# Kernel tuning notes

Hardware: AMD Instinct MI355X
Metric: run time of the kernel (lower is better)

The kernel has to match this reference:

```python
import jax, jax.numpy as jnp
import numpy as np

L, T, DIN, DOUT = 64, 8192, 128, 128

def setup_inputs() -> dict:
    key = jax.random.key(0)
    k1, k2, k3 = jax.random.split(key, 3)
    x = jax.random.normal(k1, (L, T, DIN), dtype=jnp.float32)
    w = jax.random.normal(k2, (L, DIN, DOUT), dtype=jnp.float32)
    b = jax.random.normal(k3, (L, 1, DOUT), dtype=jnp.float32)
    return {"x": x, "w": w, "b": b}

def reference(x, w, b):
    # grouped GEMM: per-layer matmul x[l] @ w[l], fused bias add
    out = jnp.einsum('lti,lio->lto', x, w) + b  # [L, T, DOUT]
    return out
```

## Files before the change

kernel.cpp:

```cpp
#include <hip/hip_runtime.h>
#include <hip/hip_bf16.h>

#define L_N 64
#define T_N 8192
#define K_N 128
#define N_N 128
#define BM  64

typedef __attribute__((ext_vector_type(8))) short short8;
typedef __attribute__((ext_vector_type(4))) float f32x4;

__device__ __forceinline__ unsigned short f2bf(float f) {
    union { float f; unsigned u; } c; c.f = f;
    return (unsigned short)((c.u + 0x7fffu + ((c.u >> 16) & 1u)) >> 16);
}

__global__ __launch_bounds__(256) void wfrag_kernel(const float* __restrict__ w,
                                                    unsigned short* __restrict__ wf) {
    __shared__ float lds[K_N * 129];
    const int l = blockIdx.x;
    const float* wl = w + (size_t)l * (K_N * N_N);
    const int tid = threadIdx.x;
    #pragma unroll
    for (int i = 0; i < 16; ++i) {
        int f = i * 256 + tid;
        float4 v = ((const float4*)wl)[f];
        int k = f >> 5, n = (f & 31) * 4;
        lds[k * 129 + n + 0] = v.x;
        lds[k * 129 + n + 1] = v.y;
        lds[k * 129 + n + 2] = v.z;
        lds[k * 129 + n + 3] = v.w;
    }
    __syncthreads();
    unsigned short* o = wf + (size_t)l * (N_N * K_N);
    #pragma unroll
    for (int c = 0; c < 16; ++c) {
        int chunk = c * 256 + tid;
        int j0   = (chunk & 1) * 4;
        int lane = (chunk >> 1) & 63;
        int kk   = (chunk >> 7) & 3;
        int ni   = chunk >> 9;
        int n  = ni * 16 + (lane & 15);
        int kb = kk * 32 + (lane >> 4) * 8 + j0;
        ushort4 ov;
        ov.x = f2bf(lds[(kb + 0) * 129 + n]);
        ov.y = f2bf(lds[(kb + 1) * 129 + n]);
        ov.z = f2bf(lds[(kb + 2) * 129 + n]);
        ov.w = f2bf(lds[(kb + 3) * 129 + n]);
        ((ushort4*)o)[chunk] = ov;
    }
}

__global__ __launch_bounds__(512, 6) void gl_kernel(const float* __restrict__ x,
                                                    const unsigned short* __restrict__ wf,
                                                    const float* __restrict__ bias,
                                                    float* __restrict__ out) {
    __shared__ __align__(16) char smem[49152];
    unsigned short* xs  = (unsigned short*)smem;
    unsigned short* wsh = (unsigned short*)(smem + 16384);

    const int tid  = threadIdx.x;
    const int lane = tid & 63;
    const int wid  = tid >> 6;
    const int lr   = lane & 15;
    const int lg   = lane >> 4;
    const int ws   = wid >> 1;
    const int ch   = wid & 1;

    const int bid  = blockIdx.x;
    const int l    = bid >> 7;
    const int tile = bid & 127;
    const float* xg = x + ((size_t)l * T_N + (size_t)tile * BM) * K_N;
    const unsigned short* wl = wf + (size_t)l * (N_N * K_N);

    #pragma unroll
    for (int i = 0; i < 4; ++i) {
        int f = i * 512 + tid;
        const float4 v = ((const float4*)xg)[f];
        int row = f >> 5;
        int kc  = (f & 31) * 4;
        union { unsigned short s[4]; unsigned long long u; } p;
        p.s[0] = f2bf(v.x); p.s[1] = f2bf(v.y); p.s[2] = f2bf(v.z); p.s[3] = f2bf(v.w);
        int us = (row * K_N + kc) ^ ((row & 7) << 3);
        *(unsigned long long*)&xs[us] = p.u;
    }
    #pragma unroll
    for (int i = 0; i < 4; ++i) {
        int c = i * 512 + tid;
        ((short8*)wsh)[c] = ((const short8*)wl)[c];
    }
    __syncthreads();

    f32x4 acc[4];
    #pragma unroll
    for (int q = 0; q < 4; ++q)
        acc[q] = (f32x4){0.f, 0.f, 0.f, 0.f};
    const int row = ws * 16 + lr;
    #pragma unroll
    for (int kk = 0; kk < 4; ++kk) {
        const short8 xb = *(const short8*)&xs[(row * K_N + kk * 32 + lg * 8) ^ ((row & 7) << 3)];
        #pragma unroll
        for (int q = 0; q < 4; ++q) {
            const int ni = ch * 4 + q;
            const short8 wv = ((const short8*)wsh)[(ni * 4 + kk) * 64 + lane];
            acc[q] = __builtin_amdgcn_mfma_f32_16x16x32_bf16(wv, xb, acc[q], 0, 0, 0);
        }
    }
    __syncthreads();

    const float* bl = bias + l * N_N;
    float4* osm = (float4*)(smem + wid * 4096);
    #pragma unroll
    for (int q = 0; q < 4; ++q) {
        const int ni = ch * 4 + q;
        const float4 bv = *(const float4*)(bl + ni * 16 + lg * 4);
        float4 r;
        r.x = acc[q][0] + bv.x;
        r.y = acc[q][1] + bv.y;
        r.z = acc[q][2] + bv.z;
        r.w = acc[q][3] + bv.w;
        osm[lr * 16 + ((q * 4 + lg) ^ lr)] = r;
    }
    float4* og4 = (float4*)(out + ((size_t)l * T_N + (size_t)tile * BM + ws * 16) * N_N);
    #pragma unroll
    for (int q2 = 0; q2 < 4; ++q2) {
        const int fi = q2 * 64 + lane;
        const int rr = fi >> 4, cc = fi & 15;
        const float4 v = osm[rr * 16 + (cc ^ rr)];
        og4[(size_t)rr * 32 + ch * 16 + cc] = v;
    }
}

extern "C" void kernel_launch(void* const* d_in, const int* in_sizes, int n_in,
                              void* d_out, int out_size, void* d_ws, size_t ws_size,
                              hipStream_t stream) {
    const float* x = (const float*)d_in[0];
    const float* w = (const float*)d_in[1];
    const float* b = (const float*)d_in[2];
    float* out = (float*)d_out;
    unsigned short* wf = (unsigned short*)d_ws;

    wfrag_kernel<<<L_N, 256, 0, stream>>>(w, wf);
    gl_kernel<<<L_N * (T_N / BM), 512, 0, stream>>>(x, wf, b, out);
}
```

Baseline: 105.8 us.

## Split output columns across two blocks per tile and remap block order

Each block now computes only half of the 128 output columns for a 64-row tile, which doubles the grid and halves the per-block weight load, LDS footprint and accumulators. Launch bounds rise to 8 blocks per CU, and block IDs are permuted so that consecutive blocks are spread across layers and tiles, possibly to match the XCD scheduling. The cost is that every x tile is now loaded from global memory and converted to bf16 twice, which adds read traffic to a memory-bound kernel.

```diff
diff --git a/kernel.cpp b/kernel.cpp
--- a/kernel.cpp
+++ b/kernel.cpp
@@ -51,11 +51,11 @@
     }
 }
 
-__global__ __launch_bounds__(512, 6) void gl_kernel(const float* __restrict__ x,
+__global__ __launch_bounds__(512, 8) void gl_kernel(const float* __restrict__ x,
                                                     const unsigned short* __restrict__ wf,
                                                     const float* __restrict__ bias,
                                                     float* __restrict__ out) {
-    __shared__ __align__(16) char smem[49152];
+    __shared__ __align__(16) char smem[32768];
     unsigned short* xs  = (unsigned short*)smem;
     unsigned short* wsh = (unsigned short*)(smem + 16384);
 
@@ -65,13 +65,15 @@
     const int lr   = lane & 15;
     const int lg   = lane >> 4;
     const int ws   = wid >> 1;
-    const int ch   = wid & 1;
+    const int cq   = wid & 1;
 
-    const int bid  = blockIdx.x;
-    const int l    = bid >> 7;
-    const int tile = bid & 127;
+    const int work = (blockIdx.x & 7) * 2048 + (blockIdx.x >> 3);
+    const int l    = work >> 8;
+    const int tile = (work & 255) >> 1;
+    const int ch   = work & 1;
+
     const float* xg = x + ((size_t)l * T_N + (size_t)tile * BM) * K_N;
-    const unsigned short* wl = wf + (size_t)l * (N_N * K_N);
+    const unsigned short* wl = wf + (size_t)l * (N_N * K_N) + (size_t)ch * 4 * 4 * 64 * 8;
 
     #pragma unroll
     for (int i = 0; i < 4; ++i) {
@@ -85,49 +87,47 @@
         *(unsigned long long*)&xs[us] = p.u;
     }
     #pragma unroll
-    for (int i = 0; i < 4; ++i) {
+    for (int i = 0; i < 2; ++i) {
         int c = i * 512 + tid;
         ((short8*)wsh)[c] = ((const short8*)wl)[c];
     }
     __syncthreads();
 
-    f32x4 acc[4];
-    #pragma unroll
-    for (int q = 0; q < 4; ++q)
-        acc[q] = (f32x4){0.f, 0.f, 0.f, 0.f};
+    f32x4 acc[2];
+    acc[0] = (f32x4){0.f, 0.f, 0.f, 0.f};
+    acc[1] = (f32x4){0.f, 0.f, 0.f, 0.f};
     const int row = ws * 16 + lr;
     #pragma unroll
     for (int kk = 0; kk < 4; ++kk) {
         const short8 xb = *(const short8*)&xs[(row * K_N + kk * 32 + lg * 8) ^ ((row & 7) << 3)];
         #pragma unroll
-        for (int q = 0; q < 4; ++q) {
-            const int ni = ch * 4 + q;
-            const short8 wv = ((const short8*)wsh)[(ni * 4 + kk) * 64 + lane];
+        for (int q = 0; q < 2; ++q) {
+            const int nl = cq * 2 + q;
+            const short8 wv = ((const short8*)wsh)[(nl * 4 + kk) * 64 + lane];
             acc[q] = __builtin_amdgcn_mfma_f32_16x16x32_bf16(wv, xb, acc[q], 0, 0, 0);
         }
     }
     __syncthreads();
 
-    const float* bl = bias + l * N_N;
-    float4* osm = (float4*)(smem + wid * 4096);
+    const float* bl = bias + l * N_N + ch * 64 + cq * 32;
+    float4* osm = (float4*)(smem + wid * 2048);
     #pragma unroll
-    for (int q = 0; q < 4; ++q) {
-        const int ni = ch * 4 + q;
-        const float4 bv = *(const float4*)(bl + ni * 16 + lg * 4);
+    for (int q = 0; q < 2; ++q) {
+        const float4 bv = *(const float4*)(bl + q * 16 + lg * 4);
         float4 r;
         r.x = acc[q][0] + bv.x;
         r.y = acc[q][1] + bv.y;
         r.z = acc[q][2] + bv.z;
         r.w = acc[q][3] + bv.w;
-        osm[lr * 16 + ((q * 4 + lg) ^ lr)] = r;
+        osm[lr * 8 + ((q * 4 + lg) ^ (lr & 7))] = r;
     }
-    float4* og4 = (float4*)(out + ((size_t)l * T_N + (size_t)tile * BM + ws * 16) * N_N);
+    float* ogb = out + ((size_t)l * T_N + (size_t)tile * BM + ws * 16) * N_N + ch * 64 + cq * 32;
     #pragma unroll
-    for (int q2 = 0; q2 < 4; ++q2) {
+    for (int q2 = 0; q2 < 2; ++q2) {
         const int fi = q2 * 64 + lane;
-        const int rr = fi >> 4, cc = fi & 15;
-        const float4 v = osm[rr * 16 + (cc ^ rr)];
-        og4[(size_t)rr * 32 + ch * 16 + cc] = v;
+        const int rr = fi >> 3, cc = fi & 7;
+        const float4 v = osm[rr * 8 + (cc ^ (rr & 7))];
+        *(float4*)(ogb + (size_t)rr * N_N + cc * 4) = v;
     }
 }
 
@@ -141,5 +141,5 @@
     unsigned short* wf = (unsigned short*)d_ws;
 
     wfrag_kernel<<<L_N, 256, 0, stream>>>(w, wf);
-    gl_kernel<<<L_N * (T_N / BM), 512, 0, stream>>>(x, wf, b, out);
+    gl_kernel<<<L_N * (T_N / BM) * 2, 512, 0, stream>>>(x, wf, b, out);
 }
```

Result: slower. 111.2 us (+5.1%).
